# Optimization experiments

Measured on AMD Instinct MI355X. Metric: run time of the kernel, lower is better.

Reference implementation:

```python
import jax, jax.numpy as jnp
import numpy as np

D_MODEL = 1024
D_FF = 4096
NUM_EXPERTS = 8
TOP_K = 2
LN_EPS = 1e-5


def setup_inputs() -> dict:
    key = jax.random.key(0)
    ks = jax.random.split(key, 12)
    B, S, D, F, E = 4, 2048, D_MODEL, D_FF, NUM_EXPERTS
    s = 0.02
    return {
        "x": jax.random.normal(ks[0], (B, S, D), jnp.float32),
        # gating network: Linear(D, D//2) -> ReLU -> Linear(D//2, E)
        "gw1": jax.random.normal(ks[1], (D, D // 2), jnp.float32) * s,
        "gb1": jnp.zeros((D // 2,), jnp.float32),
        "gw2": jax.random.normal(ks[2], (D // 2, E), jnp.float32) * s,
        "gb2": jnp.zeros((E,), jnp.float32),
        # stacked expert FFNs: Linear(D,F) -> GELU -> Linear(F,D), then *scale + bias
        "we1": jax.random.normal(ks[3], (E, D, F), jnp.float32) * s,
        "be1": jnp.zeros((E, F), jnp.float32),
        "we2": jax.random.normal(ks[4], (E, F, D), jnp.float32) * s,
        "be2": jnp.zeros((E, D), jnp.float32),
        "escale": jnp.ones((E, D), jnp.float32),
        "ebias": jax.random.normal(ks[5], (E, D), jnp.float32) * 0.01,
        # output LayerNorm
        "gamma": jnp.ones((D,), jnp.float32),
        "beta": jnp.zeros((D,), jnp.float32),
    }


def _layernorm(x, gamma, beta):
    mu = jnp.mean(x, axis=-1, keepdims=True)
    var = jnp.mean(jnp.square(x - mu), axis=-1, keepdims=True)
    return (x - mu) * jax.lax.rsqrt(var + LN_EPS) * gamma + beta


def reference(x, gw1, gb1, gw2, gb2, we1, be1, we2, be2, escale, ebias, gamma, beta):
    B, S, D = x.shape
    xf = x.reshape(-1, D)  # [T, D]

    # ---- gating (eval mode: no noise, no dropout) ----
    gate_logits = jax.nn.relu(xf @ gw1 + gb1) @ gw2 + gb2  # [T, E]
    top_v, top_i = jax.lax.top_k(gate_logits, TOP_K)       # [T, K]
    gates = jax.nn.softmax(top_v, axis=-1)                 # [T, K]

    # load balancing loss: KL( uniform || mean softmax probs ), sum reduction
    probs = jax.nn.softmax(gate_logits, axis=-1)
    expert_probs = probs.mean(axis=0)                      # [E]
    t = 1.0 / NUM_EXPERTS
    load_loss = jnp.sum(t * (jnp.log(t) - jnp.log(expert_probs + 1e-8)))

    # ---- dense compute over ALL experts (faithful to source) ----
    h = jnp.einsum('td,edf->tef', xf, we1) + be1           # [T, E, F]
    h = jax.nn.gelu(h, approximate=False)                  # nn.GELU default = erf
    eo = jnp.einsum('tef,efd->ted', h, we2) + be2          # [T, E, D]
    eo = eo * escale + ebias                               # per-expert scale/bias

    # ---- top-k gather + weighted combine ----
    sel = jnp.take_along_axis(eo, top_i[:, :, None], axis=1)  # [T, K, D]
    out = jnp.sum(gates[:, :, None] * sel, axis=1)            # [T, D]

    y = _layernorm(x + out.reshape(B, S, D), gamma, beta)
    return y, load_loss
```

## Files before the change

### kernel.cpp

```cpp
#include <hip/hip_runtime.h>
#include <hip/hip_bf16.h>
#include <math.h>

#define T_TOK 8192
#define DM    1024
#define DFF   4096
#define NE    8
#define DH    512
#define NSLOT (T_TOK*2)
#define MAXT  136

typedef float  f32x4  __attribute__((ext_vector_type(4)));
typedef __bf16 bf16x8 __attribute__((ext_vector_type(8)));

__device__ inline ushort f2bf(float f) {
  union { float f; unsigned int u; } v; v.f = f;
  unsigned int r = (v.u + 0x7FFFu + ((v.u >> 16) & 1u)) >> 16;
  return (ushort)r;
}

__device__ inline float bf2f(ushort u) {
  union { unsigned int i; float f; } v; v.i = ((unsigned int)u) << 16; return v.f;
}

__device__ __forceinline__ float gelu_erf(float v) {
  float xx = v * 0.70710678118654752f;
  float ax = fabsf(xx);
  float t  = __builtin_amdgcn_rcpf(1.f + 0.3275911f * ax);
  float p  = t * (0.254829592f + t * (-0.284496736f + t * (1.421413741f +
             t * (-1.453152027f + t * 1.061405429f))));
  float er = 1.f - p * __expf(-ax * ax);
  er = copysignf(er, xx);
  return 0.5f * v * (1.f + er);
}

__device__ inline void gl_lds16(const void* g, void* l) {
  __builtin_amdgcn_global_load_lds(
      (const __attribute__((address_space(1))) unsigned int*)g,
      (__attribute__((address_space(3))) unsigned int*)l, 16, 0, 0);
}

__global__ void k_init(int* counts, int* fill, float* psum) {
  int i = threadIdx.x;
  if (i < NE) { counts[i] = 0; fill[i] = 0; psum[i] = 0.f; }
}

__global__ void k_cvt_x(const float* __restrict__ x, ushort* __restrict__ xb, int n4) {
  int i = blockIdx.x * blockDim.x + threadIdx.x;
  int st = gridDim.x * blockDim.x;
  for (; i < n4; i += st) {
    float4 v = ((const float4*)x)[i];
    ushort4 o;
    o.x = f2bf(v.x); o.y = f2bf(v.y); o.z = f2bf(v.z); o.w = f2bf(v.w);
    ((ushort4*)xb)[i] = o;
  }
}

__global__ __launch_bounds__(256) void k_tr(const float* __restrict__ in,
                                            ushort* __restrict__ out, int R, int C) {
  __shared__ float tile[64][65];
  int e = blockIdx.z;
  in  += (size_t)e * R * C;
  out += (size_t)e * R * C;
  int r0 = blockIdx.y * 64, c0 = blockIdx.x * 64;
  int tx = threadIdx.x & 63, ty = threadIdx.x >> 6;
  for (int i = 0; i < 16; i++) {
    int r = ty + i * 4;
    tile[r][tx] = in[(size_t)(r0 + r) * C + c0 + tx];
  }
  __syncthreads();
  for (int i = 0; i < 16; i++) {
    int c = ty + i * 4;
    out[(size_t)(c0 + c) * R + r0 + tx] = f2bf(tile[tx][c]);
  }
}

__global__ __launch_bounds__(256) void k_gate1(const float* __restrict__ x,
                                               const float* __restrict__ w,
                                               const float* __restrict__ b,
                                               float* __restrict__ g1) {
  __shared__ float As[64][33];
  __shared__ float Bs[32][65];
  int m0 = blockIdx.y * 64, n0 = blockIdx.x * 64;
  int t = threadIdx.x;
  int tx = t & 15, ty = t >> 4;
  float acc[4][4] = {};
  for (int k0 = 0; k0 < DM; k0 += 32) {
#pragma unroll
    for (int i = 0; i < 2; i++) {
      int idx = t + i * 256;
      int r = idx >> 3, c4 = (idx & 7) * 4;
      float4 v = *(const float4*)&x[(size_t)(m0 + r) * DM + k0 + c4];
      As[r][c4 + 0] = v.x; As[r][c4 + 1] = v.y; As[r][c4 + 2] = v.z; As[r][c4 + 3] = v.w;
    }
#pragma unroll
    for (int i = 0; i < 2; i++) {
      int idx = t + i * 256;
      int r = idx >> 4, c4 = (idx & 15) * 4;
      float4 v = *(const float4*)&w[(size_t)(k0 + r) * DH + n0 + c4];
      Bs[r][c4 + 0] = v.x; Bs[r][c4 + 1] = v.y; Bs[r][c4 + 2] = v.z; Bs[r][c4 + 3] = v.w;
    }
    __syncthreads();
#pragma unroll
    for (int k = 0; k < 32; k++) {
      float a[4], bb[4];
#pragma unroll
      for (int i = 0; i < 4; i++) a[i] = As[ty * 4 + i][k];
#pragma unroll
      for (int j = 0; j < 4; j++) bb[j] = Bs[k][tx * 4 + j];
#pragma unroll
      for (int i = 0; i < 4; i++)
#pragma unroll
        for (int j = 0; j < 4; j++) acc[i][j] += a[i] * bb[j];
    }
    __syncthreads();
  }
#pragma unroll
  for (int i = 0; i < 4; i++)
#pragma unroll
    for (int j = 0; j < 4; j++) {
      int m = m0 + ty * 4 + i, n = n0 + tx * 4 + j;
      float v = acc[i][j] + b[n];
      g1[(size_t)m * DH + n] = fmaxf(v, 0.f);
    }
}

__global__ __launch_bounds__(256) void k_gate2(const float* __restrict__ g1,
                                               const float* __restrict__ w2,
                                               const float* __restrict__ b2,
                                               float* __restrict__ logits) {
  int wave = threadIdx.x >> 6, lane = threadIdx.x & 63;
  int tok = blockIdx.x * 4 + wave;
  const float* row = &g1[(size_t)tok * DH];
  float v[8];
#pragma unroll
  for (int j = 0; j < 8; j++) v[j] = row[lane + 64 * j];
  float acc[8];
#pragma unroll
  for (int e = 0; e < NE; e++) {
    float s = 0.f;
#pragma unroll
    for (int j = 0; j < 8; j++) s += v[j] * w2[(size_t)(lane + 64 * j) * NE + e];
    acc[e] = s;
  }
  for (int off = 32; off > 0; off >>= 1)
#pragma unroll
    for (int e = 0; e < NE; e++) acc[e] += __shfl_down(acc[e], off);
  if (lane == 0)
#pragma unroll
    for (int e = 0; e < NE; e++) logits[(size_t)tok * NE + e] = acc[e] + b2[e];
}

__global__ __launch_bounds__(256) void k_route(const float* __restrict__ logits,
                                               int* __restrict__ topi,
                                               float* __restrict__ gatesw,
                                               int* __restrict__ counts,
                                               float* __restrict__ psum) {
  int t = blockIdx.x * blockDim.x + threadIdx.x;
  const float* lp = &logits[(size_t)t * NE];
  float l[8];
#pragma unroll
  for (int e = 0; e < NE; e++) l[e] = lp[e];
  int i0 = 0; float v0 = l[0];
#pragma unroll
  for (int e = 1; e < NE; e++) if (l[e] > v0) { v0 = l[e]; i0 = e; }
  int i1 = (i0 == 0) ? 1 : 0; float v1 = l[i1];
#pragma unroll
  for (int e = 0; e < NE; e++)
    if (e != i0 && l[e] > v1) { v1 = l[e]; i1 = e; }
  float g0 = 1.f / (1.f + expf(v1 - v0));
  topi[t * 2] = i0; topi[t * 2 + 1] = i1;
  gatesw[t * 2] = g0; gatesw[t * 2 + 1] = 1.f - g0;
  float p[8]; float s = 0.f;
#pragma unroll
  for (int e = 0; e < NE; e++) { p[e] = expf(l[e] - v0); s += p[e]; }
  float inv = 1.f / s;
  int lane = threadIdx.x & 63;
#pragma unroll
  for (int e = 0; e < NE; e++) {
    float pe = p[e] * inv;
    for (int off = 32; off > 0; off >>= 1) pe += __shfl_down(pe, off);
    if (lane == 0) atomicAdd(&psum[e], pe);
  }
#pragma unroll
  for (int e = 0; e < NE; e++) {
    unsigned long long m0 = __ballot(i0 == e);
    unsigned long long m1 = __ballot(i1 == e);
    if (lane == 0) {
      int c = __popcll(m0) + __popcll(m1);
      if (c) atomicAdd(&counts[e], c);
    }
  }
}

__global__ void k_scan(const int* __restrict__ counts, int* __restrict__ offsets,
                       const float* __restrict__ psum, float* __restrict__ loss_out,
                       int* __restrict__ tile_e, int* __restrict__ tile_mt) {
  if (threadIdx.x == 0) {
    int off = 0;
    for (int e = 0; e < NE; e++) { offsets[e] = off; off += counts[e]; }
    offsets[NE] = off;
    float tt = 1.f / NE, loss = 0.f;
    for (int e = 0; e < NE; e++) {
      float pe = psum[e] / (float)T_TOK;
      loss += tt * (logf(tt) - logf(pe + 1e-8f));
    }
    loss_out[0] = loss;
    int n = 0;
    for (int e = 0; e < NE; e++) {
      int rows = counts[e];
      for (int mt = 0; mt * 128 < rows; mt++) { tile_e[n] = e; tile_mt[n] = mt; n++; }
    }
    for (int i = n; i < MAXT; i++) { tile_e[i] = -1; tile_mt[i] = 0; }
  }
}

__global__ __launch_bounds__(256) void k_fill(const int* __restrict__ topi,
                                              const int* __restrict__ offsets,
                                              int* __restrict__ fill,
                                              int* __restrict__ slot_tok,
                                              int* __restrict__ tok_slot) {
  int t = blockIdx.x * blockDim.x + threadIdx.x;
  for (int k = 0; k < 2; k++) {
    int e = topi[t * 2 + k];
    int pos = offsets[e] + atomicAdd(&fill[e], 1);
    slot_tok[pos] = t;
    tok_slot[t * 2 + k] = pos;
  }
}

__global__ __launch_bounds__(256, 3) void k_egemm1(const ushort* __restrict__ xb,
                                                   const ushort* __restrict__ w1t,
                                                   const float* __restrict__ be1,
                                                   const int* __restrict__ slot_tok,
                                                   const int* __restrict__ offsets,
                                                   const int* __restrict__ tile_e,
                                                   const int* __restrict__ tile_mt,
                                                   ushort* __restrict__ H) {
  constexpr int GX = DFF / 128;
  constexpr int NWG = GX * MAXT;
  int id = blockIdx.y * GX + blockIdx.x;
  int wg = (id & 7) * (NWG / 8) + (id >> 3);
  int ty = wg / GX;
  int n0 = (wg % GX) * 128;
  int e = tile_e[ty];
  if (e < 0) return;
  int mt = tile_mt[ty];
  int beg = offsets[e], nrows = offsets[e + 1] - beg;
  const ushort* B = w1t + (size_t)e * DFF * DM;

  __shared__ ushort As[2][4096];
  __shared__ ushort Bs[2][4096];

  int t = threadIdx.x;
  int wave = t >> 6, lane = t & 63;
  int wr = wave >> 1, wc = wave & 1;

  int r_g0 = mt * 128 + (t >> 2);
  int r_g1 = r_g0 + 64;
  int tok0 = slot_tok[beg + (r_g0 < nrows ? r_g0 : 0)];
  int tok1 = slot_tok[beg + (r_g1 < nrows ? r_g1 : 0)];
  int acol = (((t & 3) ^ ((t >> 3) & 3)) * 8);
  const ushort* aptr0 = xb + (size_t)tok0 * DM + acol;
  const ushort* aptr1 = xb + (size_t)tok1 * DM + acol;
  const ushort* bptr0 = B + (size_t)(n0 + (t >> 2)) * DM + acol;
  const ushort* bptr1 = B + (size_t)(n0 + (t >> 2) + 64) * DM + acol;
  char* adst = (char*)As + t * 16;
  char* bdst = (char*)Bs + t * 16;

  auto stage = [&](int b, int k0) {
    gl_lds16(aptr0 + k0, adst + b * 8192);
    gl_lds16(aptr1 + k0, adst + b * 8192 + 4096);
    gl_lds16(bptr0 + k0, bdst + b * 8192);
    gl_lds16(bptr1 + k0, bdst + b * 8192 + 4096);
  };

  f32x4 acc[4][4] = {};
  int la = lane & 15;
  int kqs = (((lane >> 4) ^ ((la >> 1) & 3)) * 8);
  constexpr int NT = DM / 32;

  stage(0, 0);
  stage(1, 32);
  for (int kt = 0; kt < NT; kt++) {
    if (kt + 1 < NT) asm volatile("s_waitcnt vmcnt(4)" ::: "memory");
    else             asm volatile("s_waitcnt vmcnt(0)" ::: "memory");
    __builtin_amdgcn_s_barrier();
    const ushort* Ab = As[kt & 1];
    const ushort* Bb = Bs[kt & 1];
    bf16x8 af[4], bfr[4];
#pragma unroll
    for (int m = 0; m < 4; m++)
      af[m] = *(const bf16x8*)&Ab[(wr * 64 + m * 16 + la) * 32 + kqs];
#pragma unroll
    for (int n = 0; n < 4; n++)
      bfr[n] = *(const bf16x8*)&Bb[(wc * 64 + n * 16 + la) * 32 + kqs];
    asm volatile("s_waitcnt lgkmcnt(0)" ::: "memory");
    __builtin_amdgcn_s_barrier();
    if (kt + 2 < NT) stage(kt & 1, (kt + 2) * 32);
#pragma unroll
    for (int m = 0; m < 4; m++)
#pragma unroll
      for (int n = 0; n < 4; n++)
        acc[m][n] = __builtin_amdgcn_mfma_f32_16x16x32_bf16(af[m], bfr[n], acc[m][n], 0, 0, 0);
  }

  int row0 = mt * 128 + wr * 64;
  int c_of = n0 + wc * 64;
#pragma unroll
  for (int m = 0; m < 4; m++) {
    int rbase = row0 + m * 16 + ((lane >> 4) << 2);
#pragma unroll
    for (int n = 0; n < 4; n++) {
      int c = c_of + n * 16 + la;
      float b1 = be1[e * DFF + c];
      f32x4 a = acc[m][n];
#pragma unroll
      for (int j = 0; j < 4; j++) {
        int rr = rbase + j;
        if (rr < nrows) {
          float v = a[j] + b1;
          H[(size_t)(beg + rr) * DFF + c] = f2bf(gelu_erf(v));
        }
      }
    }
  }
}

__global__ __launch_bounds__(256, 3) void k_egemm2(const ushort* __restrict__ H,
                                                   const ushort* __restrict__ w2t,
                                                   const float* __restrict__ be2,
                                                   const float* __restrict__ escale,
                                                   const float* __restrict__ ebias,
                                                   const int* __restrict__ offsets,
                                                   const int* __restrict__ tile_e,
                                                   const int* __restrict__ tile_mt,
                                                   ushort* __restrict__ eo) {
  constexpr int GX = DM / 128;
  constexpr int NWG = GX * MAXT;
  int id = blockIdx.y * GX + blockIdx.x;
  int wg = (id & 7) * (NWG / 8) + (id >> 3);
  int ty = wg / GX;
  int n0 = (wg % GX) * 128;
  int e = tile_e[ty];
  if (e < 0) return;
  int mt = tile_mt[ty];
  int beg = offsets[e], nrows = offsets[e + 1] - beg;
  const ushort* B = w2t + (size_t)e * DM * DFF;

  __shared__ ushort As[2][4096];
  __shared__ ushort Bs[2][4096];

  int t = threadIdx.x;
  int wave = t >> 6, lane = t & 63;
  int wr = wave >> 1, wc = wave & 1;

  int r_g0 = mt * 128 + (t >> 2);
  int r_g1 = r_g0 + 64;
  int s0 = beg + (r_g0 < nrows ? r_g0 : 0);
  int s1 = beg + (r_g1 < nrows ? r_g1 : 0);
  int acol = (((t & 3) ^ ((t >> 3) & 3)) * 8);
  const ushort* aptr0 = H + (size_t)s0 * DFF + acol;
  const ushort* aptr1 = H + (size_t)s1 * DFF + acol;
  const ushort* bptr0 = B + (size_t)(n0 + (t >> 2)) * DFF + acol;
  const ushort* bptr1 = B + (size_t)(n0 + (t >> 2) + 64) * DFF + acol;
  char* adst = (char*)As + t * 16;
  char* bdst = (char*)Bs + t * 16;

  auto stage = [&](int b, int k0) {
    gl_lds16(aptr0 + k0, adst + b * 8192);
    gl_lds16(aptr1 + k0, adst + b * 8192 + 4096);
    gl_lds16(bptr0 + k0, bdst + b * 8192);
    gl_lds16(bptr1 + k0, bdst + b * 8192 + 4096);
  };

  f32x4 acc[4][4] = {};
  int la = lane & 15;
  int kqs = (((lane >> 4) ^ ((la >> 1) & 3)) * 8);
  constexpr int NT = DFF / 32;

  stage(0, 0);
  stage(1, 32);
  for (int kt = 0; kt < NT; kt++) {
    if (kt + 1 < NT) asm volatile("s_waitcnt vmcnt(4)" ::: "memory");
    else             asm volatile("s_waitcnt vmcnt(0)" ::: "memory");
    __builtin_amdgcn_s_barrier();
    const ushort* Ab = As[kt & 1];
    const ushort* Bb = Bs[kt & 1];
    bf16x8 af[4], bfr[4];
#pragma unroll
    for (int m = 0; m < 4; m++)
      af[m] = *(const bf16x8*)&Ab[(wr * 64 + m * 16 + la) * 32 + kqs];
#pragma unroll
    for (int n = 0; n < 4; n++)
      bfr[n] = *(const bf16x8*)&Bb[(wc * 64 + n * 16 + la) * 32 + kqs];
    asm volatile("s_waitcnt lgkmcnt(0)" ::: "memory");
    __builtin_amdgcn_s_barrier();
    if (kt + 2 < NT) stage(kt & 1, (kt + 2) * 32);
#pragma unroll
    for (int m = 0; m < 4; m++)
#pragma unroll
      for (int n = 0; n < 4; n++)
        acc[m][n] = __builtin_amdgcn_mfma_f32_16x16x32_bf16(af[m], bfr[n], acc[m][n], 0, 0, 0);
  }

  int row0 = mt * 128 + wr * 64;
  int c_of = n0 + wc * 64;
#pragma unroll
  for (int m = 0; m < 4; m++) {
    int rbase = row0 + m * 16 + ((lane >> 4) << 2);
#pragma unroll
    for (int n = 0; n < 4; n++) {
      int c = c_of + n * 16 + la;
      float b2 = be2[e * DM + c];
      float sc = escale[e * DM + c];
      float bb = ebias[e * DM + c];
      f32x4 a = acc[m][n];
#pragma unroll
      for (int j = 0; j < 4; j++) {
        int rr = rbase + j;
        if (rr < nrows) {
          float v = (a[j] + b2) * sc + bb;
          eo[(size_t)(beg + rr) * DM + c] = f2bf(v);
        }
      }
    }
  }
}

__global__ __launch_bounds__(256) void k_ln(const float* __restrict__ x,
                                            const ushort* __restrict__ eo,
                                            const int* __restrict__ tok_slot,
                                            const float* __restrict__ gatesw,
                                            const float* __restrict__ gamma,
                                            const float* __restrict__ beta,
                                            float* __restrict__ y) {
  int t = blockIdx.x;
  int s0 = tok_slot[t * 2], s1 = tok_slot[t * 2 + 1];
  float g0 = gatesw[t * 2], g1 = gatesw[t * 2 + 1];
  const float* xr = &x[(size_t)t * DM];
  const ushort* e0 = &eo[(size_t)s0 * DM];
  const ushort* e1 = &eo[(size_t)s1 * DM];
  int tid = threadIdx.x;
  int c0 = tid * 4;
  float4 xv = *(const float4*)&xr[c0];
  ushort4 a0 = *(const ushort4*)&e0[c0];
  ushort4 a1 = *(const ushort4*)&e1[c0];
  float v[4];
  v[0] = xv.x + g0 * bf2f(a0.x) + g1 * bf2f(a1.x);
  v[1] = xv.y + g0 * bf2f(a0.y) + g1 * bf2f(a1.y);
  v[2] = xv.z + g0 * bf2f(a0.z) + g1 * bf2f(a1.z);
  v[3] = xv.w + g0 * bf2f(a0.w) + g1 * bf2f(a1.w);
  float sum = v[0] + v[1] + v[2] + v[3];
  __shared__ float red[4];
  __shared__ float red2[4];
  for (int off = 32; off > 0; off >>= 1) sum += __shfl_down(sum, off);
  if ((tid & 63) == 0) red[tid >> 6] = sum;
  __syncthreads();
  float mu = (red[0] + red[1] + red[2] + red[3]) * (1.f / DM);
  float vs = 0.f;
#pragma unroll
  for (int i = 0; i < 4; i++) { float d = v[i] - mu; vs += d * d; }
  for (int off = 32; off > 0; off >>= 1) vs += __shfl_down(vs, off);
  if ((tid & 63) == 0) red2[tid >> 6] = vs;
  __syncthreads();
  float var = (red2[0] + red2[1] + red2[2] + red2[3]) * (1.f / DM);
  float rs = rsqrtf(var + 1e-5f);
  float4 gm = *(const float4*)&gamma[c0];
  float4 bt = *(const float4*)&beta[c0];
  float4 o;
  o.x = (v[0] - mu) * rs * gm.x + bt.x;
  o.y = (v[1] - mu) * rs * gm.y + bt.y;
  o.z = (v[2] - mu) * rs * gm.z + bt.z;
  o.w = (v[3] - mu) * rs * gm.w + bt.w;
  *(float4*)&y[(size_t)t * DM + c0] = o;
}

extern "C" void kernel_launch(void* const* d_in, const int* in_sizes, int n_in,
                              void* d_out, int out_size, void* d_ws, size_t ws_size,
                              hipStream_t stream) {
  const float* x    = (const float*)d_in[0];
  const float* gw1  = (const float*)d_in[1];
  const float* gb1  = (const float*)d_in[2];
  const float* gw2  = (const float*)d_in[3];
  const float* gb2  = (const float*)d_in[4];
  const float* we1  = (const float*)d_in[5];
  const float* be1  = (const float*)d_in[6];
  const float* we2  = (const float*)d_in[7];
  const float* be2  = (const float*)d_in[8];
  const float* escale = (const float*)d_in[9];
  const float* ebias  = (const float*)d_in[10];
  const float* gamma  = (const float*)d_in[11];
  const float* beta   = (const float*)d_in[12];
  float* y = (float*)d_out;
  float* loss_out = y + (size_t)T_TOK * DM;

  char* w = (char*)d_ws;
  ushort* xb    = (ushort*)w; w += (size_t)T_TOK * DM * 2;
  ushort* w1t   = (ushort*)w; w += (size_t)NE * DFF * DM * 2;
  ushort* w2t   = (ushort*)w; w += (size_t)NE * DM * DFF * 2;
  ushort* H     = (ushort*)w; w += (size_t)NSLOT * DFF * 2;
  ushort* eo    = (ushort*)w; w += (size_t)NSLOT * DM * 2;
  float* g1     = (float*)w;  w += (size_t)T_TOK * DH * 4;
  float* logits = (float*)w;  w += (size_t)T_TOK * NE * 4;
  int*   topi   = (int*)w;    w += (size_t)T_TOK * 2 * 4;
  float* gatesw = (float*)w;  w += (size_t)T_TOK * 2 * 4;
  int* slot_tok = (int*)w;    w += (size_t)NSLOT * 4;
  int* tok_slot = (int*)w;    w += (size_t)T_TOK * 2 * 4;
  int* counts   = (int*)w;    w += 64;
  int* fill     = (int*)w;    w += 64;
  int* offsets  = (int*)w;    w += 64;
  float* psum   = (float*)w;  w += 64;
  int* tile_e   = (int*)w;    w += MAXT * 4 + 32;
  int* tile_mt  = (int*)w;    w += MAXT * 4 + 32;

  k_init<<<1, 64, 0, stream>>>(counts, fill, psum);
  k_cvt_x<<<2048, 256, 0, stream>>>(x, xb, T_TOK * DM / 4);
  k_tr<<<dim3(64, 16, 8), 256, 0, stream>>>(we1, w1t, DM, DFF);
  k_tr<<<dim3(16, 64, 8), 256, 0, stream>>>(we2, w2t, DFF, DM);
  k_gate1<<<dim3(DH / 64, T_TOK / 64), 256, 0, stream>>>(x, gw1, gb1, g1);
  k_gate2<<<T_TOK / 4, 256, 0, stream>>>(g1, gw2, gb2, logits);
  k_route<<<T_TOK / 256, 256, 0, stream>>>(logits, topi, gatesw, counts, psum);
  k_scan<<<1, 64, 0, stream>>>(counts, offsets, psum, loss_out, tile_e, tile_mt);
  k_fill<<<T_TOK / 256, 256, 0, stream>>>(topi, offsets, fill, slot_tok, tok_slot);
  k_egemm1<<<dim3(DFF / 128, MAXT), 256, 0, stream>>>(xb, w1t, be1, slot_tok, offsets,
                                                      tile_e, tile_mt, H);
  k_egemm2<<<dim3(DM / 128, MAXT), 256, 0, stream>>>(H, w2t, be2, escale, ebias,
                                                     offsets, tile_e, tile_mt, eo);
  k_ln<<<T_TOK, 256, 0, stream>>>(x, eo, tok_slot, gatesw, gamma, beta, y);
}
```

Measured before the change: 816.5 us.

## Enlarge expert GEMM tiles to 256x256 with 4-stage LDS pipeline and 8 waves

```diff
diff --git a/kernel.cpp b/kernel.cpp
--- a/kernel.cpp
+++ b/kernel.cpp
@@ -8,7 +8,7 @@
 #define NE    8
 #define DH    512
 #define NSLOT (T_TOK*2)
-#define MAXT  136
+#define MAXT2 72
 
 typedef float  f32x4  __attribute__((ext_vector_type(4)));
 typedef __bf16 bf16x8 __attribute__((ext_vector_type(8)));
@@ -39,6 +39,13 @@
       (const __attribute__((address_space(1))) unsigned int*)g,
       (__attribute__((address_space(3))) unsigned int*)l, 16, 0, 0);
 }
+
+#define VM8  asm volatile("s_waitcnt vmcnt(8)" ::: "memory")
+#define VM4  asm volatile("s_waitcnt vmcnt(4)" ::: "memory")
+#define VM0  asm volatile("s_waitcnt vmcnt(0)" ::: "memory")
+#define LGKM0 asm volatile("s_waitcnt lgkmcnt(0)" ::: "memory")
+#define SCHEDB __builtin_amdgcn_sched_barrier(0)
+#define SBAR  __builtin_amdgcn_s_barrier()
 
 __global__ void k_init(int* counts, int* fill, float* psum) {
   int i = threadIdx.x;
@@ -209,9 +216,9 @@
     int n = 0;
     for (int e = 0; e < NE; e++) {
       int rows = counts[e];
-      for (int mt = 0; mt * 128 < rows; mt++) { tile_e[n] = e; tile_mt[n] = mt; n++; }
-    }
-    for (int i = n; i < MAXT; i++) { tile_e[i] = -1; tile_mt[i] = 0; }
+      for (int mt = 0; mt * 256 < rows; mt++) { tile_e[n] = e; tile_mt[n] = mt; n++; }
+    }
+    for (int i = n; i < MAXT2; i++) { tile_e[i] = -1; tile_mt[i] = 0; }
   }
 }
 
@@ -229,7 +236,8 @@
   }
 }
 
-__global__ __launch_bounds__(256, 3) void k_egemm1(const ushort* __restrict__ xb,
+
+__global__ __launch_bounds__(512, 2) void k_egemm1(const ushort* __restrict__ xb,
                                                    const ushort* __restrict__ w1t,
                                                    const float* __restrict__ be1,
                                                    const int* __restrict__ slot_tok,
@@ -237,97 +245,128 @@
                                                    const int* __restrict__ tile_e,
                                                    const int* __restrict__ tile_mt,
                                                    ushort* __restrict__ H) {
-  constexpr int GX = DFF / 128;
-  constexpr int NWG = GX * MAXT;
+  constexpr int GX = DFF / 256;
+  constexpr int NWG = GX * MAXT2;
+  constexpr int NSLAB = DM / 32;
   int id = blockIdx.y * GX + blockIdx.x;
   int wg = (id & 7) * (NWG / 8) + (id >> 3);
   int ty = wg / GX;
-  int n0 = (wg % GX) * 128;
+  int n0 = (wg % GX) * 256;
   int e = tile_e[ty];
   if (e < 0) return;
   int mt = tile_mt[ty];
   int beg = offsets[e], nrows = offsets[e + 1] - beg;
-  const ushort* B = w1t + (size_t)e * DFF * DM;
-
-  __shared__ ushort As[2][4096];
-  __shared__ ushort Bs[2][4096];
+
+  __shared__ ushort lds[65536];
 
   int t = threadIdx.x;
-  int wave = t >> 6, lane = t & 63;
-  int wr = wave >> 1, wc = wave & 1;
-
-  int r_g0 = mt * 128 + (t >> 2);
-  int r_g1 = r_g0 + 64;
-  int tok0 = slot_tok[beg + (r_g0 < nrows ? r_g0 : 0)];
-  int tok1 = slot_tok[beg + (r_g1 < nrows ? r_g1 : 0)];
-  int acol = (((t & 3) ^ ((t >> 3) & 3)) * 8);
-  const ushort* aptr0 = xb + (size_t)tok0 * DM + acol;
-  const ushort* aptr1 = xb + (size_t)tok1 * DM + acol;
-  const ushort* bptr0 = B + (size_t)(n0 + (t >> 2)) * DM + acol;
-  const ushort* bptr1 = B + (size_t)(n0 + (t >> 2) + 64) * DM + acol;
-  char* adst = (char*)As + t * 16;
-  char* bdst = (char*)Bs + t * 16;
-
-  auto stage = [&](int b, int k0) {
-    gl_lds16(aptr0 + k0, adst + b * 8192);
-    gl_lds16(aptr1 + k0, adst + b * 8192 + 4096);
-    gl_lds16(bptr0 + k0, bdst + b * 8192);
-    gl_lds16(bptr1 + k0, bdst + b * 8192 + 4096);
-  };
-
-  f32x4 acc[4][4] = {};
-  int la = lane & 15;
-  int kqs = (((lane >> 4) ^ ((la >> 1) & 3)) * 8);
-  constexpr int NT = DM / 32;
-
-  stage(0, 0);
-  stage(1, 32);
-  for (int kt = 0; kt < NT; kt++) {
-    if (kt + 1 < NT) asm volatile("s_waitcnt vmcnt(4)" ::: "memory");
-    else             asm volatile("s_waitcnt vmcnt(0)" ::: "memory");
-    __builtin_amdgcn_s_barrier();
-    const ushort* Ab = As[kt & 1];
-    const ushort* Bb = Bs[kt & 1];
-    bf16x8 af[4], bfr[4];
-#pragma unroll
-    for (int m = 0; m < 4; m++)
-      af[m] = *(const bf16x8*)&Ab[(wr * 64 + m * 16 + la) * 32 + kqs];
-#pragma unroll
-    for (int n = 0; n < 4; n++)
-      bfr[n] = *(const bf16x8*)&Bb[(wc * 64 + n * 16 + la) * 32 + kqs];
-    asm volatile("s_waitcnt lgkmcnt(0)" ::: "memory");
-    __builtin_amdgcn_s_barrier();
-    if (kt + 2 < NT) stage(kt & 1, (kt + 2) * 32);
-#pragma unroll
-    for (int m = 0; m < 4; m++)
-#pragma unroll
-      for (int n = 0; n < 4; n++)
-        acc[m][n] = __builtin_amdgcn_mfma_f32_16x16x32_bf16(af[m], bfr[n], acc[m][n], 0, 0, 0);
-  }
-
-  int row0 = mt * 128 + wr * 64;
-  int c_of = n0 + wc * 64;
-#pragma unroll
-  for (int m = 0; m < 4; m++) {
-    int rbase = row0 + m * 16 + ((lane >> 4) << 2);
+  int lane = t & 63, lalo = lane & 15, lhi = lane >> 4;
+  int wid = t >> 6, wm = wid >> 2, wn = wid & 3;
+  int cph = lhi ^ ((lalo >> 1) & 3);
+
+  int r0 = t >> 2, r1 = r0 + 128;
+  int csrc = (t & 3) ^ ((t >> 3) & 3);
+  int ar0 = mt * 256 + r0; if (ar0 >= nrows) ar0 = nrows - 1;
+  int ar1 = mt * 256 + r1; if (ar1 >= nrows) ar1 = nrows - 1;
+  const ushort* aptr0 = xb + (size_t)slot_tok[beg + ar0] * DM + csrc * 8;
+  const ushort* aptr1 = xb + (size_t)slot_tok[beg + ar1] * DM + csrc * 8;
+  const ushort* bbase = w1t + (size_t)e * DFF * DM + csrc * 8;
+  const ushort* bptr0 = bbase + (size_t)(n0 + r0) * DM;
+  const ushort* bptr1 = bbase + (size_t)(n0 + r1) * DM;
+  ushort* ldA0 = lds + t * 8;
+  ushort* ldA1 = lds + (t + 512) * 8;
+  ushort* ldB0 = lds + 8192 + t * 8;
+  ushort* ldB1 = lds + 8192 + (t + 512) * 8;
+
+  int A_off[8], B_off[4];
+#pragma unroll
+  for (int m = 0; m < 8; m++) A_off[m] = (wm * 128 + m * 16 + lalo) * 32 + cph * 8;
+#pragma unroll
+  for (int n = 0; n < 4; n++) B_off[n] = 8192 + (wn * 64 + n * 16 + lalo) * 32 + cph * 8;
+
+  f32x4 acc[8][4] = {};
+
+#pragma unroll
+  for (int s = 0; s < 3; s++) {
+    int sl = s * 16384;
+    gl_lds16(aptr0 + s * 32, ldA0 + sl);
+    gl_lds16(bptr0 + s * 32, ldB0 + sl);
+    gl_lds16(aptr1 + s * 32, ldA1 + sl);
+    gl_lds16(bptr1 + s * 32, ldB1 + sl);
+  }
+
+  for (int s = 0; s < NSLAB; s++) {
+    int slot = (s & 3) * 16384;
+    if (s < NSLAB - 2)      { VM8; }
+    else if (s < NSLAB - 1) { VM4; }
+    else                    { VM0; }
+    SCHEDB;
+    SBAR;
+    const ushort* sb = lds + slot;
+    bf16x8 af[8], bf0, bf1, bf2, bf3;
+#pragma unroll
+    for (int m = 0; m < 8; m++) af[m] = *(const bf16x8*)(sb + A_off[m]);
+    bf0 = *(const bf16x8*)(sb + B_off[0]);
+    bf1 = *(const bf16x8*)(sb + B_off[1]);
+    if (s + 3 < NSLAB) {
+      int sl = ((s + 3) & 3) * 16384;
+      gl_lds16(aptr0 + (s + 3) * 32, ldA0 + sl);
+      gl_lds16(bptr0 + (s + 3) * 32, ldB0 + sl);
+    }
+    SBAR;
+    LGKM0; SCHEDB;
+    __builtin_amdgcn_s_setprio(1);
+#pragma unroll
+    for (int m = 0; m < 8; m++) {
+      acc[m][0] = __builtin_amdgcn_mfma_f32_16x16x32_bf16(af[m], bf0, acc[m][0], 0, 0, 0);
+      acc[m][1] = __builtin_amdgcn_mfma_f32_16x16x32_bf16(af[m], bf1, acc[m][1], 0, 0, 0);
+    }
+    __builtin_amdgcn_s_setprio(0);
+    SBAR;
+    bf2 = *(const bf16x8*)(sb + B_off[2]);
+    bf3 = *(const bf16x8*)(sb + B_off[3]);
+    if (s + 3 < NSLAB) {
+      int sl = ((s + 3) & 3) * 16384;
+      gl_lds16(aptr1 + (s + 3) * 32, ldA1 + sl);
+      gl_lds16(bptr1 + (s + 3) * 32, ldB1 + sl);
+    }
+    SBAR;
+    LGKM0; SCHEDB;
+    __builtin_amdgcn_s_setprio(1);
+#pragma unroll
+    for (int m = 0; m < 8; m++) {
+      acc[m][2] = __builtin_amdgcn_mfma_f32_16x16x32_bf16(af[m], bf2, acc[m][2], 0, 0, 0);
+      acc[m][3] = __builtin_amdgcn_mfma_f32_16x16x32_bf16(af[m], bf3, acc[m][3], 0, 0, 0);
+    }
+    __builtin_amdgcn_s_setprio(0);
+    SBAR;
+  }
+
+  int cb[4]; float b1v[4];
+#pragma unroll
+  for (int n = 0; n < 4; n++) {
+    cb[n] = n0 + wn * 64 + n * 16 + lalo;
+    b1v[n] = be1[e * DFF + cb[n]];
+  }
+#pragma unroll
+  for (int m = 0; m < 8; m++) {
+    int lrow = wm * 128 + m * 16 + lhi * 4;
 #pragma unroll
     for (int n = 0; n < 4; n++) {
-      int c = c_of + n * 16 + la;
-      float b1 = be1[e * DFF + c];
       f32x4 a = acc[m][n];
 #pragma unroll
       for (int j = 0; j < 4; j++) {
-        int rr = rbase + j;
+        int rr = mt * 256 + lrow + j;
         if (rr < nrows) {
-          float v = a[j] + b1;
-          H[(size_t)(beg + rr) * DFF + c] = f2bf(gelu_erf(v));
+          float v = a[j] + b1v[n];
+          H[(size_t)(beg + rr) * DFF + cb[n]] = f2bf(gelu_erf(v));
         }
       }
     }
   }
 }
 
-__global__ __launch_bounds__(256, 3) void k_egemm2(const ushort* __restrict__ H,
+__global__ __launch_bounds__(512, 2) void k_egemm2(const ushort* __restrict__ H,
                                                    const ushort* __restrict__ w2t,
                                                    const float* __restrict__ be2,
                                                    const float* __restrict__ escale,
@@ -336,92 +375,123 @@
                                                    const int* __restrict__ tile_e,
                                                    const int* __restrict__ tile_mt,
                                                    ushort* __restrict__ eo) {
-  constexpr int GX = DM / 128;
-  constexpr int NWG = GX * MAXT;
+  constexpr int GX = DM / 256;
+  constexpr int NWG = GX * MAXT2;
+  constexpr int NSLAB = DFF / 32;
   int id = blockIdx.y * GX + blockIdx.x;
   int wg = (id & 7) * (NWG / 8) + (id >> 3);
   int ty = wg / GX;
-  int n0 = (wg % GX) * 128;
+  int n0 = (wg % GX) * 256;
   int e = tile_e[ty];
   if (e < 0) return;
   int mt = tile_mt[ty];
   int beg = offsets[e], nrows = offsets[e + 1] - beg;
-  const ushort* B = w2t + (size_t)e * DM * DFF;
-
-  __shared__ ushort As[2][4096];
-  __shared__ ushort Bs[2][4096];
+
+  __shared__ ushort lds[65536];
 
   int t = threadIdx.x;
-  int wave = t >> 6, lane = t & 63;
-  int wr = wave >> 1, wc = wave & 1;
-
-  int r_g0 = mt * 128 + (t >> 2);
-  int r_g1 = r_g0 + 64;
-  int s0 = beg + (r_g0 < nrows ? r_g0 : 0);
-  int s1 = beg + (r_g1 < nrows ? r_g1 : 0);
-  int acol = (((t & 3) ^ ((t >> 3) & 3)) * 8);
-  const ushort* aptr0 = H + (size_t)s0 * DFF + acol;
-  const ushort* aptr1 = H + (size_t)s1 * DFF + acol;
-  const ushort* bptr0 = B + (size_t)(n0 + (t >> 2)) * DFF + acol;
-  const ushort* bptr1 = B + (size_t)(n0 + (t >> 2) + 64) * DFF + acol;
-  char* adst = (char*)As + t * 16;
-  char* bdst = (char*)Bs + t * 16;
-
-  auto stage = [&](int b, int k0) {
-    gl_lds16(aptr0 + k0, adst + b * 8192);
-    gl_lds16(aptr1 + k0, adst + b * 8192 + 4096);
-    gl_lds16(bptr0 + k0, bdst + b * 8192);
-    gl_lds16(bptr1 + k0, bdst + b * 8192 + 4096);
-  };
-
-  f32x4 acc[4][4] = {};
-  int la = lane & 15;
-  int kqs = (((lane >> 4) ^ ((la >> 1) & 3)) * 8);
-  constexpr int NT = DFF / 32;
-
-  stage(0, 0);
-  stage(1, 32);
-  for (int kt = 0; kt < NT; kt++) {
-    if (kt + 1 < NT) asm volatile("s_waitcnt vmcnt(4)" ::: "memory");
-    else             asm volatile("s_waitcnt vmcnt(0)" ::: "memory");
-    __builtin_amdgcn_s_barrier();
-    const ushort* Ab = As[kt & 1];
-    const ushort* Bb = Bs[kt & 1];
-    bf16x8 af[4], bfr[4];
-#pragma unroll
-    for (int m = 0; m < 4; m++)
-      af[m] = *(const bf16x8*)&Ab[(wr * 64 + m * 16 + la) * 32 + kqs];
-#pragma unroll
-    for (int n = 0; n < 4; n++)
-      bfr[n] = *(const bf16x8*)&Bb[(wc * 64 + n * 16 + la) * 32 + kqs];
-    asm volatile("s_waitcnt lgkmcnt(0)" ::: "memory");
-    __builtin_amdgcn_s_barrier();
-    if (kt + 2 < NT) stage(kt & 1, (kt + 2) * 32);
-#pragma unroll
-    for (int m = 0; m < 4; m++)
-#pragma unroll
-      for (int n = 0; n < 4; n++)
-        acc[m][n] = __builtin_amdgcn_mfma_f32_16x16x32_bf16(af[m], bfr[n], acc[m][n], 0, 0, 0);
-  }
-
-  int row0 = mt * 128 + wr * 64;
-  int c_of = n0 + wc * 64;
-#pragma unroll
-  for (int m = 0; m < 4; m++) {
-    int rbase = row0 + m * 16 + ((lane >> 4) << 2);
+  int lane = t & 63, lalo = lane & 15, lhi = lane >> 4;
+  int wid = t >> 6, wm = wid >> 2, wn = wid & 3;
+  int cph = lhi ^ ((lalo >> 1) & 3);
+
+  int r0 = t >> 2, r1 = r0 + 128;
+  int csrc = (t & 3) ^ ((t >> 3) & 3);
+  int ar0 = mt * 256 + r0; if (ar0 >= nrows) ar0 = nrows - 1;
+  int ar1 = mt * 256 + r1; if (ar1 >= nrows) ar1 = nrows - 1;
+  const ushort* aptr0 = H + (size_t)(beg + ar0) * DFF + csrc * 8;
+  const ushort* aptr1 = H + (size_t)(beg + ar1) * DFF + csrc * 8;
+  const ushort* bbase = w2t + (size_t)e * DM * DFF + csrc * 8;
+  const ushort* bptr0 = bbase + (size_t)(n0 + r0) * DFF;
+  const ushort* bptr1 = bbase + (size_t)(n0 + r1) * DFF;
+  ushort* ldA0 = lds + t * 8;
+  ushort* ldA1 = lds + (t + 512) * 8;
+  ushort* ldB0 = lds + 8192 + t * 8;
+  ushort* ldB1 = lds + 8192 + (t + 512) * 8;
+
+  int A_off[8], B_off[4];
+#pragma unroll
+  for (int m = 0; m < 8; m++) A_off[m] = (wm * 128 + m * 16 + lalo) * 32 + cph * 8;
+#pragma unroll
+  for (int n = 0; n < 4; n++) B_off[n] = 8192 + (wn * 64 + n * 16 + lalo) * 32 + cph * 8;
+
+  f32x4 acc[8][4] = {};
+
+#pragma unroll
+  for (int s = 0; s < 3; s++) {
+    int sl = s * 16384;
+    gl_lds16(aptr0 + s * 32, ldA0 + sl);
+    gl_lds16(bptr0 + s * 32, ldB0 + sl);
+    gl_lds16(aptr1 + s * 32, ldA1 + sl);
+    gl_lds16(bptr1 + s * 32, ldB1 + sl);
+  }
+
+  for (int s = 0; s < NSLAB; s++) {
+    int slot = (s & 3) * 16384;
+    if (s < NSLAB - 2)      { VM8; }
+    else if (s < NSLAB - 1) { VM4; }
+    else                    { VM0; }
+    SCHEDB;
+    SBAR;
+    const ushort* sb = lds + slot;
+    bf16x8 af[8], bf0, bf1, bf2, bf3;
+#pragma unroll
+    for (int m = 0; m < 8; m++) af[m] = *(const bf16x8*)(sb + A_off[m]);
+    bf0 = *(const bf16x8*)(sb + B_off[0]);
+    bf1 = *(const bf16x8*)(sb + B_off[1]);
+    if (s + 3 < NSLAB) {
+      int sl = ((s + 3) & 3) * 16384;
+      gl_lds16(aptr0 + (s + 3) * 32, ldA0 + sl);
+      gl_lds16(bptr0 + (s + 3) * 32, ldB0 + sl);
+    }
+    SBAR;
+    LGKM0; SCHEDB;
+    __builtin_amdgcn_s_setprio(1);
+#pragma unroll
+    for (int m = 0; m < 8; m++) {
+      acc[m][0] = __builtin_amdgcn_mfma_f32_16x16x32_bf16(af[m], bf0, acc[m][0], 0, 0, 0);
+      acc[m][1] = __builtin_amdgcn_mfma_f32_16x16x32_bf16(af[m], bf1, acc[m][1], 0, 0, 0);
+    }
+    __builtin_amdgcn_s_setprio(0);
+    SBAR;
+    bf2 = *(const bf16x8*)(sb + B_off[2]);
+    bf3 = *(const bf16x8*)(sb + B_off[3]);
+    if (s + 3 < NSLAB) {
+      int sl = ((s + 3) & 3) * 16384;
+      gl_lds16(aptr1 + (s + 3) * 32, ldA1 + sl);
+      gl_lds16(bptr1 + (s + 3) * 32, ldB1 + sl);
+    }
+    SBAR;
+    LGKM0; SCHEDB;
+    __builtin_amdgcn_s_setprio(1);
+#pragma unroll
+    for (int m = 0; m < 8; m++) {
+      acc[m][2] = __builtin_amdgcn_mfma_f32_16x16x32_bf16(af[m], bf2, acc[m][2], 0, 0, 0);
+      acc[m][3] = __builtin_amdgcn_mfma_f32_16x16x32_bf16(af[m], bf3, acc[m][3], 0, 0, 0);
+    }
+    __builtin_amdgcn_s_setprio(0);
+    SBAR;
+  }
+
+  int cb[4]; float b2v[4], scv[4], bbv[4];
+#pragma unroll
+  for (int n = 0; n < 4; n++) {
+    cb[n] = n0 + wn * 64 + n * 16 + lalo;
+    b2v[n] = be2[e * DM + cb[n]];
+    scv[n] = escale[e * DM + cb[n]];
+    bbv[n] = ebias[e * DM + cb[n]];
+  }
+#pragma unroll
+  for (int m = 0; m < 8; m++) {
+    int lrow = wm * 128 + m * 16 + lhi * 4;
 #pragma unroll
     for (int n = 0; n < 4; n++) {
-      int c = c_of + n * 16 + la;
-      float b2 = be2[e * DM + c];
-      float sc = escale[e * DM + c];
-      float bb = ebias[e * DM + c];
       f32x4 a = acc[m][n];
 #pragma unroll
       for (int j = 0; j < 4; j++) {
-        int rr = rbase + j;
+        int rr = mt * 256 + lrow + j;
         if (rr < nrows) {
-          float v = (a[j] + b2) * sc + bb;
-          eo[(size_t)(beg + rr) * DM + c] = f2bf(v);
+          float v = (a[j] + b2v[n]) * scv[n] + bbv[n];
+          eo[(size_t)(beg + rr) * DM + cb[n]] = f2bf(v);
         }
       }
     }
@@ -511,8 +581,8 @@
   int* fill     = (int*)w;    w += 64;
   int* offsets  = (int*)w;    w += 64;
   float* psum   = (float*)w;  w += 64;
-  int* tile_e   = (int*)w;    w += MAXT * 4 + 32;
-  int* tile_mt  = (int*)w;    w += MAXT * 4 + 32;
+  int* tile_e   = (int*)w;    w += MAXT2 * 4 + 32;
+  int* tile_mt  = (int*)w;    w += MAXT2 * 4 + 32;
 
   k_init<<<1, 64, 0, stream>>>(counts, fill, psum);
   k_cvt_x<<<2048, 256, 0, stream>>>(x, xb, T_TOK * DM / 4);
@@ -523,9 +593,9 @@
   k_route<<<T_TOK / 256, 256, 0, stream>>>(logits, topi, gatesw, counts, psum);
   k_scan<<<1, 64, 0, stream>>>(counts, offsets, psum, loss_out, tile_e, tile_mt);
   k_fill<<<T_TOK / 256, 256, 0, stream>>>(topi, offsets, fill, slot_tok, tok_slot);
-  k_egemm1<<<dim3(DFF / 128, MAXT), 256, 0, stream>>>(xb, w1t, be1, slot_tok, offsets,
-                                                      tile_e, tile_mt, H);
-  k_egemm2<<<dim3(DM / 128, MAXT), 256, 0, stream>>>(H, w2t, be2, escale, ebias,
-                                                     offsets, tile_e, tile_mt, eo);
+  k_egemm1<<<dim3(DFF / 256, MAXT2), 512, 0, stream>>>(xb, w1t, be1, slot_tok, offsets,
+                                                       tile_e, tile_mt, H);
+  k_egemm2<<<dim3(DM / 256, MAXT2), 512, 0, stream>>>(H, w2t, be2, escale, ebias,
+                                                      offsets, tile_e, tile_mt, eo);
   k_ln<<<T_TOK, 256, 0, stream>>>(x, eo, tok_slot, gatesw, gamma, beta, y);
 }
```

Result: slower. 913.8 us (+11.9%).

## Run gating GEMM on MFMA with split-bf16 (hi/lo) emulation of fp32

Applied to the files above, without the earlier changes.

```diff
diff --git a/kernel.cpp b/kernel.cpp
--- a/kernel.cpp
+++ b/kernel.cpp
@@ -45,14 +45,19 @@
   if (i < NE) { counts[i] = 0; fill[i] = 0; psum[i] = 0.f; }
 }
 
-__global__ void k_cvt_x(const float* __restrict__ x, ushort* __restrict__ xb, int n4) {
+__global__ void k_cvt_x(const float* __restrict__ x, ushort* __restrict__ xh,
+                        ushort* __restrict__ xl, int n4) {
   int i = blockIdx.x * blockDim.x + threadIdx.x;
   int st = gridDim.x * blockDim.x;
   for (; i < n4; i += st) {
     float4 v = ((const float4*)x)[i];
-    ushort4 o;
-    o.x = f2bf(v.x); o.y = f2bf(v.y); o.z = f2bf(v.z); o.w = f2bf(v.w);
-    ((ushort4*)xb)[i] = o;
+    ushort4 h, l;
+    h.x = f2bf(v.x); l.x = f2bf(v.x - bf2f(h.x));
+    h.y = f2bf(v.y); l.y = f2bf(v.y - bf2f(h.y));
+    h.z = f2bf(v.z); l.z = f2bf(v.z - bf2f(h.z));
+    h.w = f2bf(v.w); l.w = f2bf(v.w - bf2f(h.w));
+    ((ushort4*)xh)[i] = h;
+    ((ushort4*)xl)[i] = l;
   }
 }
 
@@ -75,54 +80,126 @@
   }
 }
 
-__global__ __launch_bounds__(256) void k_gate1(const float* __restrict__ x,
-                                               const float* __restrict__ w,
-                                               const float* __restrict__ b,
-                                               float* __restrict__ g1) {
-  __shared__ float As[64][33];
-  __shared__ float Bs[32][65];
-  int m0 = blockIdx.y * 64, n0 = blockIdx.x * 64;
+__global__ __launch_bounds__(256) void k_trg(const float* __restrict__ in,
+                                             ushort* __restrict__ outh,
+                                             ushort* __restrict__ outl) {
+  __shared__ float tile[64][65];
+  int r0 = blockIdx.y * 64, c0 = blockIdx.x * 64;
+  int tx = threadIdx.x & 63, ty = threadIdx.x >> 6;
+  for (int i = 0; i < 16; i++) {
+    int r = ty + i * 4;
+    tile[r][tx] = in[(size_t)(r0 + r) * DH + c0 + tx];
+  }
+  __syncthreads();
+  for (int i = 0; i < 16; i++) {
+    int c = ty + i * 4;
+    float f = tile[tx][c];
+    ushort h = f2bf(f);
+    outh[(size_t)(c0 + c) * DM + r0 + tx] = h;
+    outl[(size_t)(c0 + c) * DM + r0 + tx] = f2bf(f - bf2f(h));
+  }
+}
+
+__global__ __launch_bounds__(256) void k_gate1m(const ushort* __restrict__ xh,
+                                                const ushort* __restrict__ xl,
+                                                const ushort* __restrict__ w1ht,
+                                                const ushort* __restrict__ w1lt,
+                                                const float* __restrict__ b,
+                                                float* __restrict__ g1) {
+  constexpr int GX = DH / 128;
+  constexpr int NWG = GX * (T_TOK / 128);
+  int id = blockIdx.y * GX + blockIdx.x;
+  int wg = (id & 7) * (NWG / 8) + (id >> 3);
+  int m0 = (wg / GX) * 128;
+  int n0 = (wg % GX) * 128;
+
+  __shared__ ushort lds[2][16384];
+
   int t = threadIdx.x;
-  int tx = t & 15, ty = t >> 4;
-  float acc[4][4] = {};
-  for (int k0 = 0; k0 < DM; k0 += 32) {
-#pragma unroll
-    for (int i = 0; i < 2; i++) {
-      int idx = t + i * 256;
-      int r = idx >> 3, c4 = (idx & 7) * 4;
-      float4 v = *(const float4*)&x[(size_t)(m0 + r) * DM + k0 + c4];
-      As[r][c4 + 0] = v.x; As[r][c4 + 1] = v.y; As[r][c4 + 2] = v.z; As[r][c4 + 3] = v.w;
-    }
-#pragma unroll
-    for (int i = 0; i < 2; i++) {
-      int idx = t + i * 256;
-      int r = idx >> 4, c4 = (idx & 15) * 4;
-      float4 v = *(const float4*)&w[(size_t)(k0 + r) * DH + n0 + c4];
-      Bs[r][c4 + 0] = v.x; Bs[r][c4 + 1] = v.y; Bs[r][c4 + 2] = v.z; Bs[r][c4 + 3] = v.w;
-    }
-    __syncthreads();
-#pragma unroll
-    for (int k = 0; k < 32; k++) {
-      float a[4], bb[4];
-#pragma unroll
-      for (int i = 0; i < 4; i++) a[i] = As[ty * 4 + i][k];
-#pragma unroll
-      for (int j = 0; j < 4; j++) bb[j] = Bs[k][tx * 4 + j];
-#pragma unroll
-      for (int i = 0; i < 4; i++)
-#pragma unroll
-        for (int j = 0; j < 4; j++) acc[i][j] += a[i] * bb[j];
-    }
-    __syncthreads();
-  }
-#pragma unroll
-  for (int i = 0; i < 4; i++)
-#pragma unroll
-    for (int j = 0; j < 4; j++) {
-      int m = m0 + ty * 4 + i, n = n0 + tx * 4 + j;
-      float v = acc[i][j] + b[n];
-      g1[(size_t)m * DH + n] = fmaxf(v, 0.f);
-    }
+  int wave = t >> 6, lane = t & 63;
+  int wr = wave >> 1, wc = wave & 1;
+
+  int r = t >> 2;
+  int csrc = (((t & 3) ^ ((t >> 3) & 3)) * 8);
+  const ushort* ah0 = xh + (size_t)(m0 + r) * DM + csrc;
+  const ushort* ah1 = xh + (size_t)(m0 + r + 64) * DM + csrc;
+  const ushort* al0 = xl + (size_t)(m0 + r) * DM + csrc;
+  const ushort* al1 = xl + (size_t)(m0 + r + 64) * DM + csrc;
+  const ushort* bh0 = w1ht + (size_t)(n0 + r) * DM + csrc;
+  const ushort* bh1 = w1ht + (size_t)(n0 + r + 64) * DM + csrc;
+  const ushort* bl0 = w1lt + (size_t)(n0 + r) * DM + csrc;
+  const ushort* bl1 = w1lt + (size_t)(n0 + r + 64) * DM + csrc;
+
+  auto stage = [&](int b_, int k0) {
+    ushort* base = lds[b_];
+    gl_lds16(ah0 + k0, base + t * 8);
+    gl_lds16(ah1 + k0, base + (t + 256) * 8);
+    gl_lds16(al0 + k0, base + 4096 + t * 8);
+    gl_lds16(al1 + k0, base + 4096 + (t + 256) * 8);
+    gl_lds16(bh0 + k0, base + 8192 + t * 8);
+    gl_lds16(bh1 + k0, base + 8192 + (t + 256) * 8);
+    gl_lds16(bl0 + k0, base + 12288 + t * 8);
+    gl_lds16(bl1 + k0, base + 12288 + (t + 256) * 8);
+  };
+
+  f32x4 acc[4][4] = {};
+  int la = lane & 15;
+  int kqs = (((lane >> 4) ^ ((la >> 1) & 3)) * 8);
+  constexpr int NT = DM / 32;
+
+  stage(0, 0);
+  stage(1, 32);
+  for (int kt = 0; kt < NT; kt++) {
+    if (kt + 1 < NT) asm volatile("s_waitcnt vmcnt(8)" ::: "memory");
+    else             asm volatile("s_waitcnt vmcnt(0)" ::: "memory");
+    __builtin_amdgcn_s_barrier();
+    const ushort* bb = lds[kt & 1];
+    bf16x8 fah[4], fal[4], fbh[4], fbl[4];
+#pragma unroll
+    for (int m = 0; m < 4; m++) {
+      int ro = (wr * 64 + m * 16 + la) * 32 + kqs;
+      fah[m] = *(const bf16x8*)&bb[ro];
+      fal[m] = *(const bf16x8*)&bb[4096 + ro];
+    }
+#pragma unroll
+    for (int n = 0; n < 4; n++) {
+      int ro = (wc * 64 + n * 16 + la) * 32 + kqs;
+      fbh[n] = *(const bf16x8*)&bb[8192 + ro];
+      fbl[n] = *(const bf16x8*)&bb[12288 + ro];
+    }
+    asm volatile("s_waitcnt lgkmcnt(0)" ::: "memory");
+    __builtin_amdgcn_s_barrier();
+    if (kt + 2 < NT) stage(kt & 1, (kt + 2) * 32);
+#pragma unroll
+    for (int m = 0; m < 4; m++)
+#pragma unroll
+      for (int n = 0; n < 4; n++)
+        acc[m][n] = __builtin_amdgcn_mfma_f32_16x16x32_bf16(fah[m], fbh[n], acc[m][n], 0, 0, 0);
+#pragma unroll
+    for (int m = 0; m < 4; m++)
+#pragma unroll
+      for (int n = 0; n < 4; n++)
+        acc[m][n] = __builtin_amdgcn_mfma_f32_16x16x32_bf16(fah[m], fbl[n], acc[m][n], 0, 0, 0);
+#pragma unroll
+    for (int m = 0; m < 4; m++)
+#pragma unroll
+      for (int n = 0; n < 4; n++)
+        acc[m][n] = __builtin_amdgcn_mfma_f32_16x16x32_bf16(fal[m], fbh[n], acc[m][n], 0, 0, 0);
+  }
+
+#pragma unroll
+  for (int m = 0; m < 4; m++) {
+    int rbase = m0 + wr * 64 + m * 16 + ((lane >> 4) << 2);
+#pragma unroll
+    for (int n = 0; n < 4; n++) {
+      int c = n0 + wc * 64 + n * 16 + la;
+      float bv = b[c];
+      f32x4 a = acc[m][n];
+#pragma unroll
+      for (int j = 0; j < 4; j++)
+        g1[(size_t)(rbase + j) * DH + c] = fmaxf(a[j] + bv, 0.f);
+    }
+  }
 }
 
 __global__ __launch_bounds__(256) void k_gate2(const float* __restrict__ g1,
@@ -496,11 +573,14 @@
   float* loss_out = y + (size_t)T_TOK * DM;
 
   char* w = (char*)d_ws;
-  ushort* xb    = (ushort*)w; w += (size_t)T_TOK * DM * 2;
+  ushort* xh    = (ushort*)w; w += (size_t)T_TOK * DM * 2;
+  ushort* xl    = (ushort*)w; w += (size_t)T_TOK * DM * 2;
   ushort* w1t   = (ushort*)w; w += (size_t)NE * DFF * DM * 2;
   ushort* w2t   = (ushort*)w; w += (size_t)NE * DM * DFF * 2;
   ushort* H     = (ushort*)w; w += (size_t)NSLOT * DFF * 2;
   ushort* eo    = (ushort*)w; w += (size_t)NSLOT * DM * 2;
+  ushort* w1ht  = (ushort*)w; w += (size_t)DH * DM * 2;
+  ushort* w1lt  = (ushort*)w; w += (size_t)DH * DM * 2;
   float* g1     = (float*)w;  w += (size_t)T_TOK * DH * 4;
   float* logits = (float*)w;  w += (size_t)T_TOK * NE * 4;
   int*   topi   = (int*)w;    w += (size_t)T_TOK * 2 * 4;
@@ -515,15 +595,16 @@
   int* tile_mt  = (int*)w;    w += MAXT * 4 + 32;
 
   k_init<<<1, 64, 0, stream>>>(counts, fill, psum);
-  k_cvt_x<<<2048, 256, 0, stream>>>(x, xb, T_TOK * DM / 4);
+  k_cvt_x<<<2048, 256, 0, stream>>>(x, xh, xl, T_TOK * DM / 4);
+  k_trg<<<dim3(8, 16), 256, 0, stream>>>(gw1, w1ht, w1lt);
   k_tr<<<dim3(64, 16, 8), 256, 0, stream>>>(we1, w1t, DM, DFF);
   k_tr<<<dim3(16, 64, 8), 256, 0, stream>>>(we2, w2t, DFF, DM);
-  k_gate1<<<dim3(DH / 64, T_TOK / 64), 256, 0, stream>>>(x, gw1, gb1, g1);
+  k_gate1m<<<dim3(DH / 128, T_TOK / 128), 256, 0, stream>>>(xh, xl, w1ht, w1lt, gb1, g1);
   k_gate2<<<T_TOK / 4, 256, 0, stream>>>(g1, gw2, gb2, logits);
   k_route<<<T_TOK / 256, 256, 0, stream>>>(logits, topi, gatesw, counts, psum);
   k_scan<<<1, 64, 0, stream>>>(counts, offsets, psum, loss_out, tile_e, tile_mt);
   k_fill<<<T_TOK / 256, 256, 0, stream>>>(topi, offsets, fill, slot_tok, tok_slot);
-  k_egemm1<<<dim3(DFF / 128, MAXT), 256, 0, stream>>>(xb, w1t, be1, slot_tok, offsets,
+  k_egemm1<<<dim3(DFF / 128, MAXT), 256, 0, stream>>>(xh, w1t, be1, slot_tok, offsets,
                                                       tile_e, tile_mt, H);
   k_egemm2<<<dim3(DM / 128, MAXT), 256, 0, stream>>>(H, w2t, be2, escale, ebias,
                                                      offsets, tile_e, tile_mt, eo);
```

Measured after the change: 688.8 us. 15.6% less time.
